# Kernel tuning notes

Measured on AMD Instinct MI355X. Metric: run time of the kernel, lower is better.

The kernel has to match this reference:

```python
import jax, jax.numpy as jnp
import numpy as np

EXP_ORDER = 2  # matches init_kwargs exp_order
N_FEAT = 8
Q_DIM = 1
BATCH = 262144
T_EXPANDED = 164  # n + C(n+1,2) + C(n+2,3) for n=8, degrees 1..3
N_OUT = 8


def taylor_expand(x, exp_order):
    """Faithful vectorized version of the nested multiply/concat loop.

    x: [B, n, q]. Builds all monomials of degree 1..exp_order+1 using the same
    recursion as the TF code: at each order, for each j, multiply x_j with the
    previous-order block starting at Id[j], then append. The q-loop in the
    original is replaced by broadcasting over the q axis (identical math).
    """
    n = x.shape[1]
    Id = list(range(n))  # start index of x_j's block in the previous-order terms
    epd = x
    for _ in range(exp_order):
        L = epd.shape[1]  # slice end Id[n-1]+1 always equals current length
        blocks = []
        new_Id = []
        offset = L
        for j in range(n):
            blk = x[:, j:j + 1, :] * epd[:, Id[j]:L, :]  # [B, L-Id[j], q]
            new_Id.append(offset)
            offset += blk.shape[1]
            blocks.append(blk)
        epd = jnp.concatenate([epd] + blocks, axis=1)
        Id = new_Id
    return epd


def setup_inputs() -> dict:
    key = jax.random.key(0)
    k1, k2, k3 = jax.random.split(key, 3)
    x = jax.random.normal(k1, (BATCH, N_FEAT, Q_DIM), dtype=jnp.float32)
    # 'dl' init: uniform(-1/sqrt(fan), 1/sqrt(fan)) with fan = weights_shape[0]
    dl_scale = 1.0 / np.sqrt(N_OUT)
    W = jax.random.uniform(k2, (N_OUT, T_EXPANDED), minval=-dl_scale,
                           maxval=dl_scale, dtype=jnp.float32)
    # 'uniform' bias init: U(-0.2, 0.2), shape [out, 1]
    b = jax.random.uniform(k3, (N_OUT, 1), minval=-0.2, maxval=0.2,
                           dtype=jnp.float32)
    return {"x": x, "W": W, "b": b}


def reference(x, W, b):
    # cp_type == 'none': pass-through of the input
    epd = taylor_expand(x, EXP_ORDER)          # [B, T, q]
    out = jnp.einsum('ot,btq->boq', W, epd) + b[None]  # [B, out, q]
    # act_type == 'relu'
    return jax.nn.relu(out)
```

## Files before the change

### kernel.cpp

```cpp
#include <hip/hip_runtime.h>
#include <hip/hip_bf16.h>
#include <string.h>


static constexpr int TEXP = 164;
static constexpr int NOUT = 8;
static constexpr int NMFMA = 11;
static constexpr int NSLOT = 88;
static constexpr int BIAS_T = 200;
static constexpr int NWP = NMFMA * 64 * 8;

using f32x16 = __attribute__((ext_vector_type(16))) float;
using short8 = __attribute__((ext_vector_type(8))) short;

constexpr int rowstart2(int j) { return j * 8 - j * (j - 1) / 2; }
constexpr int start3(int j) {
  int s = 44;
  for (int jp = 0; jp < j; ++jp) s += (8 - jp) * (9 - jp) / 2;
  return s;
}
constexpr int t3_of(int a, int b, int c) {
  int x = a, y = b, z = c, t = 0;
  if (x > y) { t = x; x = y; y = t; }
  if (y > z) { t = y; y = z; z = t; }
  if (x > y) { t = x; x = y; y = t; }
  int off = 0;
  for (int ap = x; ap < y; ++ap) off += 8 - ap;
  return start3(x) + off + (z - y);
}

struct Slot { int deg, a, b, c; };
struct SlotTable { Slot s[NSLOT]; };

constexpr bool isrep2(int j, int k) {
  if (k < 4) return true;
  if (j >= 4) return false;
  if (k == j + 4) return true;
  return j < k - 4;
}
constexpr bool isrep3(int a, int b, int c) {
  return ((a < 4) + (b < 4) + (c < 4)) >= 2;
}

constexpr SlotTable make_slots() {
  SlotTable T{};
  int s = 0;
  for (int j = 0; j < 4; ++j) T.s[s++] = {1, j, 0, 0};
  for (int j = 0; j < 8; ++j)
    for (int k = j; k < 8; ++k)
      if (isrep2(j, k)) T.s[s++] = {2, j, k, 0};
  for (int a = 0; a < 8; ++a)
    for (int b = a; b < 8; ++b)
      for (int c = b; c < 8; ++c)
        if (isrep3(a, b, c)) T.s[s++] = {3, a, b, c};
  for (; s < NSLOT; ++s) T.s[s] = {0, 0, 0, 0};
  return T;
}
constexpr SlotTable SLOTS = make_slots();

struct TT { short t[2][NSLOT]; };
constexpr TT make_tt() {
  TT r{};
  for (int h = 0; h < 2; ++h)
    for (int s = 0; s < NSLOT; ++s) {
      Slot sl = SLOTS.s[s];
      int m = h ? 4 : 0;
      if (sl.deg == 0) {
        r.t[h][s] = (short)((h == 0 && s == 84) ? BIAS_T : -1);
      } else if (sl.deg == 1) {
        r.t[h][s] = (short)(sl.a ^ m);
      } else if (sl.deg == 2) {
        if (h == 1 && sl.b == (sl.a ^ 4)) { r.t[h][s] = -1; }
        else {
          int a = sl.a ^ m, b = sl.b ^ m;
          int lo = a < b ? a : b, hi2 = a < b ? b : a;
          r.t[h][s] = (short)(8 + rowstart2(lo) + (hi2 - lo));
        }
      } else {
        r.t[h][s] = (short)t3_of(sl.a ^ m, sl.b ^ m, sl.c ^ m);
      }
    }
  return r;
}
__device__ const TT TDX = make_tt();

__device__ __forceinline__ unsigned short bf16rne(float v) {
  union { float f; unsigned int u; } c; c.f = v;
  unsigned int u = c.u;
  return (unsigned short)((u + 0x7fffu + ((u >> 16) & 1u)) >> 16);
}

template <int S>
__device__ __forceinline__ float slotval(const float (&xs)[8], const float (&d2)[36]) {
  constexpr int deg = SLOTS.s[S].deg;
  constexpr int a = SLOTS.s[S].a;
  constexpr int b = SLOTS.s[S].b;
  constexpr int c = SLOTS.s[S].c;
  if constexpr (deg == 1) return xs[a];
  else if constexpr (deg == 2) return d2[rowstart2(a) + (b - a)];
  else if constexpr (deg == 3) return xs[a] * d2[rowstart2(b) + (c - b)];
  else if constexpr (S == 84) return 1.0f;
  else return 0.0f;
}

template <int I>
struct MfmaStep {
  static __device__ __forceinline__ void run(const float (&xs)[8], const float (&d2)[36],
                                             const unsigned short* wlds_lane,
                                             short8 af_cur, f32x16& acc) {
    short8 af_next;
    if constexpr (I + 1 < NMFMA)
      af_next = *reinterpret_cast<const short8*>(wlds_lane + (I + 1) * 64 * 8);
    short8 bv;
    bv[0] = (short)bf16rne(slotval<8 * I + 0>(xs, d2));
    bv[1] = (short)bf16rne(slotval<8 * I + 1>(xs, d2));
    bv[2] = (short)bf16rne(slotval<8 * I + 2>(xs, d2));
    bv[3] = (short)bf16rne(slotval<8 * I + 3>(xs, d2));
    bv[4] = (short)bf16rne(slotval<8 * I + 4>(xs, d2));
    bv[5] = (short)bf16rne(slotval<8 * I + 5>(xs, d2));
    bv[6] = (short)bf16rne(slotval<8 * I + 6>(xs, d2));
    bv[7] = (short)bf16rne(slotval<8 * I + 7>(xs, d2));
    acc = __builtin_amdgcn_mfma_f32_32x32x16_bf16(af_cur, bv, acc, 0, 0, 0);
    if constexpr (I + 1 < NMFMA)
      MfmaStep<I + 1>::run(xs, d2, wlds_lane, af_next, acc);
  }
};

__global__ __launch_bounds__(256, 4) void taylor_mfma(
    const float* __restrict__ x, const float* __restrict__ W,
    const float* __restrict__ b, float* __restrict__ out, int ngroups) {
  __shared__ __align__(16) unsigned short wlds[NWP];

  for (int k = (int)threadIdx.x; k < NWP; k += 256) {
    int j = k & 7;
    int lane = (k >> 3) & 63;
    int i = k >> 9;
    int row = lane & 31, h = lane >> 5;
    int t = TDX.t[h][8 * i + j];
    float v = 0.0f;
    if (row < NOUT) {
      if (t >= 0 && t < TEXP) v = W[row * TEXP + t];
      else if (t == BIAS_T) v = b[row];
    }
    wlds[k] = bf16rne(v);
  }
  __syncthreads();

  const int lane = (int)(threadIdx.x & 63);
  const int h = (lane >= 32) ? 1 : 0;
  const int col = lane & 31;

  const int g = (int)((blockIdx.x * blockDim.x + threadIdx.x) >> 6);
  if (g >= ngroups) return;
  const int elem = g * 32 + col;

  const float* xe = x + elem * 8;
  float4 fA = *reinterpret_cast<const float4*>(xe + 4 * h);
  float4 fB = *reinterpret_cast<const float4*>(xe + 4 - 4 * h);
  float xs[8] = {fA.x, fA.y, fA.z, fA.w, fB.x, fB.y, fB.z, fB.w};

  const unsigned short* wlds_lane = wlds + lane * 8;
  short8 af0 = *reinterpret_cast<const short8*>(wlds_lane);

  float d2[36];
#pragma unroll
  for (int j = 0; j < 4; ++j) {
#pragma unroll
    for (int k = j; k < 8; ++k) {
      d2[rowstart2(j) + (k - j)] = xs[j] * xs[k];
    }
  }

  f32x16 acc;
#pragma unroll
  for (int r = 0; r < 16; ++r) acc[r] = 0.0f;

  MfmaStep<0>::run(xs, d2, wlds_lane, af0, acc);

  float4 o;
  o.x = fmaxf(acc[0], 0.0f);
  o.y = fmaxf(acc[1], 0.0f);
  o.z = fmaxf(acc[2], 0.0f);
  o.w = fmaxf(acc[3], 0.0f);
  *reinterpret_cast<float4*>(out + elem * 8 + 4 * h) = o;
}

extern "C" void kernel_launch(void* const* d_in, const int* in_sizes, int n_in,
                              void* d_out, int out_size, void* d_ws, size_t ws_size,
                              hipStream_t stream) {
  const float* x = (const float*)d_in[0];
  const float* W = (const float*)d_in[1];
  const float* b = (const float*)d_in[2];
  float* out = (float*)d_out;

  int n = in_sizes[0] / 8;
  int ngroups = n / 32;
  int blocks = ngroups / 4;

  taylor_mfma<<<blocks, 256, 0, stream>>>(x, W, b, out, ngroups);
}
```

Baseline: 17.46 us.

## Pack weights in a separate prep kernel and process two groups per wave

Moves the bf16 weight packing out of each block's LDS preamble into a small prep kernel that writes to workspace, and the main kernel then reads weight fragments straight from global/L2 instead of LDS. Each wave now handles two 32-element groups, which halves the block count and spreads the per-wave setup over more work. The d2 array is trimmed to its 26 used entries. This adds a second kernel launch and turns LDS weight reads into global loads, which may add latency per MFMA step.

```diff
diff --git a/kernel.cpp b/kernel.cpp
--- a/kernel.cpp
+++ b/kernel.cpp
@@ -91,7 +91,7 @@
 }
 
 template <int S>
-__device__ __forceinline__ float slotval(const float (&xs)[8], const float (&d2)[36]) {
+__device__ __forceinline__ float slotval(const float (&xs)[8], const float (&d2)[26]) {
   constexpr int deg = SLOTS.s[S].deg;
   constexpr int a = SLOTS.s[S].a;
   constexpr int b = SLOTS.s[S].b;
@@ -105,12 +105,12 @@
 
 template <int I>
 struct MfmaStep {
-  static __device__ __forceinline__ void run(const float (&xs)[8], const float (&d2)[36],
-                                             const unsigned short* wlds_lane,
+  static __device__ __forceinline__ void run(const float (&xs)[8], const float (&d2)[26],
+                                             const unsigned short* __restrict__ wpl,
                                              short8 af_cur, f32x16& acc) {
     short8 af_next;
     if constexpr (I + 1 < NMFMA)
-      af_next = *reinterpret_cast<const short8*>(wlds_lane + (I + 1) * 64 * 8);
+      af_next = *reinterpret_cast<const short8*>(wpl + (I + 1) * 64 * 8);
     short8 bv;
     bv[0] = (short)bf16rne(slotval<8 * I + 0>(xs, d2));
     bv[1] = (short)bf16rne(slotval<8 * I + 1>(xs, d2));
@@ -122,47 +122,14 @@
     bv[7] = (short)bf16rne(slotval<8 * I + 7>(xs, d2));
     acc = __builtin_amdgcn_mfma_f32_32x32x16_bf16(af_cur, bv, acc, 0, 0, 0);
     if constexpr (I + 1 < NMFMA)
-      MfmaStep<I + 1>::run(xs, d2, wlds_lane, af_next, acc);
+      MfmaStep<I + 1>::run(xs, d2, wpl, af_next, acc);
   }
 };
 
-__global__ __launch_bounds__(256, 4) void taylor_mfma(
-    const float* __restrict__ x, const float* __restrict__ W,
-    const float* __restrict__ b, float* __restrict__ out, int ngroups) {
-  __shared__ __align__(16) unsigned short wlds[NWP];
-
-  for (int k = (int)threadIdx.x; k < NWP; k += 256) {
-    int j = k & 7;
-    int lane = (k >> 3) & 63;
-    int i = k >> 9;
-    int row = lane & 31, h = lane >> 5;
-    int t = TDX.t[h][8 * i + j];
-    float v = 0.0f;
-    if (row < NOUT) {
-      if (t >= 0 && t < TEXP) v = W[row * TEXP + t];
-      else if (t == BIAS_T) v = b[row];
-    }
-    wlds[k] = bf16rne(v);
-  }
-  __syncthreads();
-
-  const int lane = (int)(threadIdx.x & 63);
-  const int h = (lane >= 32) ? 1 : 0;
-  const int col = lane & 31;
-
-  const int g = (int)((blockIdx.x * blockDim.x + threadIdx.x) >> 6);
-  if (g >= ngroups) return;
-  const int elem = g * 32 + col;
-
-  const float* xe = x + elem * 8;
-  float4 fA = *reinterpret_cast<const float4*>(xe + 4 * h);
-  float4 fB = *reinterpret_cast<const float4*>(xe + 4 - 4 * h);
-  float xs[8] = {fA.x, fA.y, fA.z, fA.w, fB.x, fB.y, fB.z, fB.w};
-
-  const unsigned short* wlds_lane = wlds + lane * 8;
-  short8 af0 = *reinterpret_cast<const short8*>(wlds_lane);
-
-  float d2[36];
+__device__ __forceinline__ void chain(const float (&xs)[8],
+                                      const unsigned short* __restrict__ wpl,
+                                      float* __restrict__ dst) {
+  float d2[26];
 #pragma unroll
   for (int j = 0; j < 4; ++j) {
 #pragma unroll
@@ -170,19 +137,64 @@
       d2[rowstart2(j) + (k - j)] = xs[j] * xs[k];
     }
   }
-
+  short8 af0 = *reinterpret_cast<const short8*>(wpl);
   f32x16 acc;
 #pragma unroll
   for (int r = 0; r < 16; ++r) acc[r] = 0.0f;
-
-  MfmaStep<0>::run(xs, d2, wlds_lane, af0, acc);
-
+  MfmaStep<0>::run(xs, d2, wpl, af0, acc);
   float4 o;
   o.x = fmaxf(acc[0], 0.0f);
   o.y = fmaxf(acc[1], 0.0f);
   o.z = fmaxf(acc[2], 0.0f);
   o.w = fmaxf(acc[3], 0.0f);
-  *reinterpret_cast<float4*>(out + elem * 8 + 4 * h) = o;
+  *reinterpret_cast<float4*>(dst) = o;
+}
+
+__global__ void prep_w(const float* __restrict__ W, const float* __restrict__ b,
+                       unsigned short* __restrict__ wp) {
+  int idx = threadIdx.x + blockIdx.x * blockDim.x;
+  if (idx >= NWP) return;
+  int j = idx & 7;
+  int lane = (idx >> 3) & 63;
+  int i = idx >> 9;
+  int row = lane & 31, h = lane >> 5;
+  int t = TDX.t[h][8 * i + j];
+  float v = 0.0f;
+  if (row < NOUT) {
+    if (t >= 0 && t < TEXP) v = W[row * TEXP + t];
+    else if (t == BIAS_T) v = b[row];
+  }
+  wp[idx] = bf16rne(v);
+}
+
+__global__ __launch_bounds__(256, 4) void taylor_mfma(
+    const float* __restrict__ x, const unsigned short* __restrict__ wp,
+    float* __restrict__ out, int ngroups) {
+  const int lane = (int)(threadIdx.x & 63);
+  const int h = (lane >= 32) ? 1 : 0;
+  const int col = lane & 31;
+
+  const int wave = (int)((blockIdx.x * blockDim.x + threadIdx.x) >> 6);
+  const int g0 = wave * 2;
+  if (g0 >= ngroups) return;
+
+  const int elem0 = g0 * 32 + col;
+  const int elem1 = elem0 + 32;
+
+  const float* xe0 = x + elem0 * 8;
+  const float* xe1 = x + elem1 * 8;
+  float4 a0 = *reinterpret_cast<const float4*>(xe0 + 4 * h);
+  float4 b0 = *reinterpret_cast<const float4*>(xe0 + 4 - 4 * h);
+  float4 a1 = *reinterpret_cast<const float4*>(xe1 + 4 * h);
+  float4 b1 = *reinterpret_cast<const float4*>(xe1 + 4 - 4 * h);
+
+  const unsigned short* wpl = wp + lane * 8;
+
+  float xs0[8] = {a0.x, a0.y, a0.z, a0.w, b0.x, b0.y, b0.z, b0.w};
+  chain(xs0, wpl, out + elem0 * 8 + 4 * h);
+
+  float xs1[8] = {a1.x, a1.y, a1.z, a1.w, b1.x, b1.y, b1.z, b1.w};
+  chain(xs1, wpl, out + elem1 * 8 + 4 * h);
 }
 
 extern "C" void kernel_launch(void* const* d_in, const int* in_sizes, int n_in,
@@ -192,10 +204,12 @@
   const float* W = (const float*)d_in[1];
   const float* b = (const float*)d_in[2];
   float* out = (float*)d_out;
+  unsigned short* wp = (unsigned short*)d_ws;
 
   int n = in_sizes[0] / 8;
   int ngroups = n / 32;
-  int blocks = ngroups / 4;
-
-  taylor_mfma<<<blocks, 256, 0, stream>>>(x, W, b, out, ngroups);
-}
+  int blocks = ngroups / 8;
+
+  prep_w<<<22, 256, 0, stream>>>(W, b, wp);
+  taylor_mfma<<<blocks, 256, 0, stream>>>(x, wp, out, ngroups);
+}
```

New measurement: 17.25 us. No clear change (-1.2%).
